# Optimization experiments

Measured on AMD Instinct MI355X. Metric: run time of the kernel, lower is better.

## Reference

```python
import jax, jax.numpy as jnp
import numpy as np

K = 20
EPS = 1e-5
NEG_SLOPE = 0.2


def knn(x, k):
    # x: [B, C, N] -> idx [B, N, k] of nearest neighbors (negative sq-dist topk)
    inner = -2.0 * jnp.einsum('bcn,bcm->bnm', x, x)
    xx = jnp.sum(x * x, axis=1)  # [B, N]
    d = -xx[:, :, None] - inner - xx[:, None, :]
    return jax.lax.top_k(d, k)[1]


def get_graph_feature(x, k):
    # x: [B, C, N] -> [B, 2C, N, k]
    idx = knn(x, k)
    xt = jnp.transpose(x, (0, 2, 1))            # [B, N, C]
    feat = jax.vmap(lambda a, i: a[i])(xt, idx)  # [B, N, k, C]
    center = xt[:, :, None, :]
    out = jnp.concatenate([feat - center, jnp.broadcast_to(center, feat.shape)], axis=-1)
    return jnp.transpose(out, (0, 3, 1, 2))


def conv_bn_lrelu(x, w, g, b):
    # 1x1 conv + BatchNorm2d (batch stats, training mode) + LeakyReLU(0.2)
    y = jnp.einsum('oc,bcnk->bonk', w, x)
    mu = jnp.mean(y, axis=(0, 2, 3), keepdims=True)
    var = jnp.mean((y - mu) ** 2, axis=(0, 2, 3), keepdims=True)
    y = (y - mu) * jax.lax.rsqrt(var + EPS)
    y = y * g[None, :, None, None] + b[None, :, None, None]
    return jnp.where(y >= 0, y, NEG_SLOPE * y)


def lrelu(y):
    return jnp.where(y >= 0, y, NEG_SLOPE * y)


def setup_inputs() -> dict:
    key = jax.random.key(0)
    ks = jax.random.split(key, 24)
    B, N = 8, 4096
    d = {}
    d['x'] = jax.random.normal(ks[0], (B, 3, N), dtype=jnp.float32)
    def wconv(k_, o, c):
        return jax.random.normal(k_, (o, c), dtype=jnp.float32) * (1.0 / np.sqrt(c))
    d['w1'] = wconv(ks[1], 32, 6)
    d['g1'] = 1.0 + 0.1 * jax.random.normal(ks[2], (32,), dtype=jnp.float32)
    d['b1'] = 0.1 * jax.random.normal(ks[3], (32,), dtype=jnp.float32)
    d['w2'] = wconv(ks[4], 64, 70)
    d['g2'] = 1.0 + 0.1 * jax.random.normal(ks[5], (64,), dtype=jnp.float32)
    d['b2'] = 0.1 * jax.random.normal(ks[6], (64,), dtype=jnp.float32)
    d['wd1'] = wconv(ks[7], 64, 64)
    d['gd1'] = 1.0 + 0.1 * jax.random.normal(ks[8], (64,), dtype=jnp.float32)
    d['bd1'] = 0.1 * jax.random.normal(ks[9], (64,), dtype=jnp.float32)
    d['wd2'] = wconv(ks[10], 64, 128)
    d['gd2'] = 1.0 + 0.1 * jax.random.normal(ks[11], (64,), dtype=jnp.float32)
    d['bd2'] = 0.1 * jax.random.normal(ks[12], (64,), dtype=jnp.float32)
    d['W2d'] = jax.random.normal(ks[13], (128, 128), dtype=jnp.float32) * (1.0 / np.sqrt(128))
    d['b2d'] = 0.1 * jax.random.normal(ks[14], (128,), dtype=jnp.float32)
    d['W3d'] = jax.random.normal(ks[15], (64, 128), dtype=jnp.float32) * (1.0 / np.sqrt(128))
    d['b3d'] = 0.1 * jax.random.normal(ks[16], (64,), dtype=jnp.float32)
    d['W4d'] = jax.random.normal(ks[17], (11, 64), dtype=jnp.float32) * (1.0 / np.sqrt(64))
    d['b4d'] = 0.1 * jax.random.normal(ks[18], (11,), dtype=jnp.float32)
    return d


def reference(x, w1, g1, b1, w2, g2, b2, wd1, gd1, bd1, wd2, gd2, bd2,
              W2d, b2d, W3d, b3d, W4d, b4d):
    x1_gf = get_graph_feature(x, K)                    # [B, 6, N, k]
    x1_max = jnp.max(conv_bn_lrelu(x1_gf, w1, g1, b1), axis=-1)  # [B, 32, N]
    x2_gf = jnp.concatenate([x1_gf, get_graph_feature(x1_max, K)], axis=1)  # [B, 70, N, k]
    x2_max = jnp.max(conv_bn_lrelu(x2_gf, w2, g2, b2), axis=-1)  # [B, 64, N]
    xd1 = jnp.max(conv_bn_lrelu(get_graph_feature(x1_max, K), wd1, gd1, bd1), axis=-1)  # [B, 64, N]
    xd2 = jnp.max(conv_bn_lrelu(get_graph_feature(x2_max, K), wd2, gd2, bd2), axis=-1)  # [B, 64, N]
    h = jnp.concatenate([xd1, xd2], axis=1)            # [B, 128, N]
    h = h.reshape(1, -1, 128)                          # faithful row-major view
    h = jnp.mean(h, axis=1)                            # [1, 128]
    h = lrelu(h @ W2d.T + b2d)
    h = lrelu(h @ W3d.T + b3d)
    return lrelu(h @ W4d.T + b4d)                      # [1, 11]
```

## Files before the change

### kernel.cpp

```cpp
#include <hip/hip_runtime.h>

#define BB 8
#define NN 4096
#define KK 20
constexpr float EPSV = 1e-5f;
constexpr float SLOPE = 0.2f;

typedef __bf16 bfrag __attribute__((ext_vector_type(8)));
typedef float floatx4 __attribute__((ext_vector_type(4)));
typedef unsigned short us4 __attribute__((ext_vector_type(4)));

__device__ __forceinline__ float lrelu(float v) { return v >= 0.f ? v : SLOPE * v; }

__device__ __forceinline__ unsigned short bf16rn(float f) {
    unsigned int u = __float_as_uint(f);
    return (unsigned short)((u + 0x7FFFu + ((u >> 16) & 1u)) >> 16);
}
__device__ __forceinline__ float bf16up(unsigned short h) {
    return __uint_as_float(((unsigned int)h) << 16);
}

__global__ void zero_kernel(float* p, int n) {
    int i = blockIdx.x * 256 + threadIdx.x;
    if (i < n) p[i] = 0.f;
}

template<int C>
__global__ void halfnorm_kernel(const float* __restrict__ src, float* __restrict__ hng) {
    int n = blockIdx.x * 256 + threadIdx.x;
    int b = blockIdx.y;
    float s = 0.f;
    #pragma unroll
    for (int c = 0; c < C; c++) { float v = src[(b * C + c) * NN + n]; s += v * v; }
    hng[b * NN + n] = 0.5f * s;
}

template<int C>
__global__ __launch_bounds__(256) void knn_kernel(const float* __restrict__ src,
                                                  const float* __restrict__ hng,
                                                  int* __restrict__ idx) {
    constexpr int SK = (C == 3) ? 40 : (2 * C + 8);
    __shared__ unsigned short qpack[64 * SK];
    __shared__ unsigned short cpack[64 * SK];
    __shared__ float hn[64];
    __shared__ float pv[64 * 65];
    __shared__ unsigned short pidx[64 * 66];
    __shared__ float tau[64];
    __shared__ int   cnt[64];

    const int b = blockIdx.y;
    const int q0 = blockIdx.x * 64;
    const int tid = threadIdx.x;
    const int lane = tid & 63;
    const int wv = tid >> 6;
    const int wr = (wv >> 1) * 32;
    const int wc = (wv & 1) * 32;
    const int fl = lane & 15;
    const int fq = lane >> 4;

    if (C == 3) {
        for (int i = tid; i < 64 * 20; i += 256) {
            int r = i / 20, k = 12 + i % 20;
            qpack[r * SK + k] = 0; cpack[r * SK + k] = 0;
        }
        if (tid < 64) {
            int q = tid;
            #pragma unroll
            for (int c = 0; c < 3; c++) {
                float v = src[(b * 3 + c) * NN + q0 + q];
                unsigned short h = bf16rn(v);
                unsigned short l = bf16rn(v - bf16up(h));
                qpack[q * SK + c] = h;  qpack[q * SK + 3 + c] = l;
                qpack[q * SK + 6 + c] = h;  qpack[q * SK + 9 + c] = l;
            }
        }
    } else {
        for (int t = 0; t < C / 16; t++) {
            int i = t * 256 + tid;
            int c4 = (i >> 6) * 4, m = i & 63;
            us4 hv, lv;
            #pragma unroll
            for (int j = 0; j < 4; j++) {
                float v = src[(b * C + c4 + j) * NN + q0 + m];
                unsigned short h = bf16rn(v);
                hv[j] = h;
                lv[j] = bf16rn(v - bf16up(h));
            }
            *(us4*)(&qpack[m * SK + c4]) = hv;
            *(us4*)(&qpack[m * SK + C + c4]) = lv;
        }
    }
    if (tid < 64) { tau[tid] = -3.4e38f; cnt[tid] = 0; }

    float tv[20]; int ti[20];
    #pragma unroll
    for (int k = 0; k < 20; k++) { tv[k] = -3.4e38f; ti[k] = 0; }
    __syncthreads();

    for (int ch = 0; ch < 64; ch++) {
        const int m0 = ch * 64;
        if (C == 3) {
            if (tid < 64) {
                int m = tid;
                #pragma unroll
                for (int c = 0; c < 3; c++) {
                    float v = src[(b * 3 + c) * NN + m0 + m];
                    unsigned short h = bf16rn(v);
                    unsigned short l = bf16rn(v - bf16up(h));
                    cpack[m * SK + c] = h;  cpack[m * SK + 3 + c] = l;
                    cpack[m * SK + 6 + c] = l;  cpack[m * SK + 9 + c] = h;
                }
            }
        } else {
            for (int t = 0; t < C / 16; t++) {
                int i = t * 256 + tid;
                int c4 = (i >> 6) * 4, m = i & 63;
                us4 hv, lv;
                #pragma unroll
                for (int j = 0; j < 4; j++) {
                    float v = src[(b * C + c4 + j) * NN + m0 + m];
                    unsigned short h = bf16rn(v);
                    hv[j] = h;
                    lv[j] = bf16rn(v - bf16up(h));
                }
                *(us4*)(&cpack[m * SK + c4]) = hv;
                *(us4*)(&cpack[m * SK + C + c4]) = lv;
            }
        }
        if (tid < 16) *(float4*)(hn + tid * 4) = *(const float4*)(hng + b * NN + m0 + tid * 4);
        __syncthreads();

        floatx4 acc[2][2];
        #pragma unroll
        for (int r2 = 0; r2 < 2; r2++)
            #pragma unroll
            for (int c2 = 0; c2 < 2; c2++)
                acc[r2][c2] = (floatx4)(0.f);

        if (C == 3) {
            #pragma unroll
            for (int r2 = 0; r2 < 2; r2++) {
                bfrag a = *(const bfrag*)(&qpack[(wr + r2 * 16 + fl) * SK + fq * 8]);
                #pragma unroll
                for (int c2 = 0; c2 < 2; c2++) {
                    bfrag bm = *(const bfrag*)(&cpack[(wc + c2 * 16 + fl) * SK + fq * 8]);
                    acc[r2][c2] = __builtin_amdgcn_mfma_f32_16x16x32_bf16(a, bm, acc[r2][c2], 0, 0, 0);
                }
            }
        } else {
            #pragma unroll
            for (int kk = 0; kk < C / 32; kk++) {
                const int kb = kk * 32 + fq * 8;
                bfrag ah[2], al[2], bh[2], bl[2];
                #pragma unroll
                for (int r2 = 0; r2 < 2; r2++) {
                    ah[r2] = *(const bfrag*)(&qpack[(wr + r2 * 16 + fl) * SK + kb]);
                    al[r2] = *(const bfrag*)(&qpack[(wr + r2 * 16 + fl) * SK + C + kb]);
                }
                #pragma unroll
                for (int c2 = 0; c2 < 2; c2++) {
                    bh[c2] = *(const bfrag*)(&cpack[(wc + c2 * 16 + fl) * SK + kb]);
                    bl[c2] = *(const bfrag*)(&cpack[(wc + c2 * 16 + fl) * SK + C + kb]);
                }
                #pragma unroll
                for (int r2 = 0; r2 < 2; r2++)
                    #pragma unroll
                    for (int c2 = 0; c2 < 2; c2++) {
                        acc[r2][c2] = __builtin_amdgcn_mfma_f32_16x16x32_bf16(ah[r2], bh[c2], acc[r2][c2], 0, 0, 0);
                        acc[r2][c2] = __builtin_amdgcn_mfma_f32_16x16x32_bf16(ah[r2], bl[c2], acc[r2][c2], 0, 0, 0);
                        acc[r2][c2] = __builtin_amdgcn_mfma_f32_16x16x32_bf16(al[r2], bh[c2], acc[r2][c2], 0, 0, 0);
                        acc[r2][c2] = __builtin_amdgcn_mfma_f32_16x16x32_bf16(al[r2], bl[c2], acc[r2][c2], 0, 0, 0);
                    }
            }
        }

        float hnv[2];
        #pragma unroll
        for (int c2 = 0; c2 < 2; c2++) hnv[c2] = hn[wc + c2 * 16 + fl];
        #pragma unroll
        for (int r2 = 0; r2 < 2; r2++) {
            float4 t4 = *(const float4*)(&tau[wr + r2 * 16 + fq * 4]);
            float ta[4] = {t4.x, t4.y, t4.z, t4.w};
            #pragma unroll
            for (int c2 = 0; c2 < 2; c2++) {
                #pragma unroll
                for (int reg = 0; reg < 4; reg++) {
                    float s = acc[r2][c2][reg] - hnv[c2];
                    if (s > ta[reg]) {
                        int q = wr + r2 * 16 + fq * 4 + reg;
                        int p = atomicAdd(&cnt[q], 1);
                        pv[q * 65 + p] = s;
                        pidx[q * 66 + p] = (unsigned short)(m0 + wc + c2 * 16 + fl);
                    }
                }
            }
        }
        __syncthreads();

        if (tid < 64) {
            int n = cnt[tid];
            for (int t = 0; t < n; t++) {
                float v = pv[tid * 65 + t];
                if (v > tv[0]) {
                    tv[0] = v; ti[0] = (int)pidx[tid * 66 + t];
                    #pragma unroll
                    for (int j = 0; j < 19; j++) {
                        if (tv[j] > tv[j + 1]) {
                            float a = tv[j]; tv[j] = tv[j + 1]; tv[j + 1] = a;
                            int bi = ti[j]; ti[j] = ti[j + 1]; ti[j + 1] = bi;
                        }
                    }
                }
            }
            cnt[tid] = 0;
            tau[tid] = tv[0];
        }
        __syncthreads();
    }

    if (tid < 64) {
        #pragma unroll
        for (int k = 0; k < 20; k++)
            idx[(b * NN + q0 + tid) * KK + k] = ti[k];
    }
}

template<int COUT>
__global__ void precompute_kernel(const float* __restrict__ src, int C,
                                  const float* __restrict__ w, int CIN, int wd_off, int wc_off,
                                  float* __restrict__ G, float* __restrict__ H,
                                  int initG, int initH) {
    constexpr int MY = 256 / COUT;
    extern __shared__ float lds[];
    float* wd = lds;
    float* wc = lds + C * COUT;
    const int b = blockIdx.y;
    const int tid = threadIdx.y * COUT + threadIdx.x;
    for (int i = tid; i < C * COUT; i += 256) {
        int c = i / COUT, o = i % COUT;
        float a  = w[o * CIN + wd_off + c];
        float cc = w[o * CIN + wc_off + c];
        wd[i] = a;
        wc[i] = cc - a;
    }
    __syncthreads();
    const int o = threadIdx.x;
    for (int it = 0; it < COUT / 4; it++) {
        int m = blockIdx.x * 64 + it * MY + threadIdx.y;
        float g = 0.f, h = 0.f;
        for (int c = 0; c < C; c++) {
            float s = src[(b * C + c) * NN + m];
            g += wd[c * COUT + o] * s;
            h += wc[c * COUT + o] * s;
        }
        int gi = (b * NN + m) * COUT + o;
        if (initG) G[gi] = g; else G[gi] += g;
        if (initH) H[gi] = h; else H[gi] += h;
    }
}

template<int COUT, int GROUPS>
__global__ void conv_stats_kernel(const float* __restrict__ G1, const int* __restrict__ idx1,
                                  const float* __restrict__ G2, const int* __restrict__ idx2,
                                  const float* __restrict__ H, float* __restrict__ stats,
                                  float* __restrict__ MaxY, float* __restrict__ MinY) {
    constexpr int NY = 256 / COUT;
    const int b = blockIdx.y;
    const int o = threadIdx.x;
    const int n = blockIdx.x * NY + threadIdx.y;
    const int base = b * NN + n;
    const float h = H[base * COUT + o];
    float s1 = 0.f, s2 = 0.f;
    float gx = -3.4e38f, gn = 3.4e38f;
    #pragma unroll
    for (int k = 0; k < KK; k++) {
        int i1 = idx1[base * KK + k];
        float g = G1[(b * NN + i1) * COUT + o];
        if (GROUPS == 2) {
            int i2 = idx2[base * KK + k];
            g += G2[(b * NN + i2) * COUT + o];
        }
        float y = g + h;
        s1 += y;
        s2 += y * y;
        gx = fmaxf(gx, g);
        gn = fminf(gn, g);
    }
    MaxY[base * COUT + o] = gx + h;
    MinY[base * COUT + o] = gn + h;

    __shared__ float ls[2 * COUT];
    if (threadIdx.y == 0) { ls[o] = 0.f; ls[COUT + o] = 0.f; }
    __syncthreads();
    atomicAdd(&ls[o], s1);
    atomicAdd(&ls[COUT + o], s2);
    __syncthreads();
    if (threadIdx.y == 0) {
        atomicAdd(&stats[o], ls[o]);
        atomicAdd(&stats[64 + o], ls[COUT + o]);
    }
}

__global__ void finalize_kernel(const float* __restrict__ g, const float* __restrict__ bb,
                                float* __restrict__ stats, int cout, float invP) {
    int o = threadIdx.x;
    if (o >= cout) return;
    float mu  = stats[o] * invP;
    float var = stats[64 + o] * invP - mu * mu;
    float sc  = g[o] * rsqrtf(var + EPSV);
    stats[128 + o] = sc;
    stats[192 + o] = bb[o] - mu * sc;
}

__global__ void apply_kernel(const float* __restrict__ MaxY, const float* __restrict__ MinY,
                             const float* __restrict__ stats, float* __restrict__ out, int cout) {
    int e = blockIdx.x * 256 + threadIdx.x;
    int total = BB * cout * NN;
    if (e >= total) return;
    int n = e & (NN - 1);
    int o = (e >> 12) % cout;
    int b = e / (NN * cout);
    float sc = stats[128 + o], sh = stats[192 + o];
    int si = (b * NN + n) * cout + o;
    float v = (sc >= 0.f) ? MaxY[si] : MinY[si];
    out[e] = lrelu(sc * v + sh);
}

__global__ void mean_kernel(const float* __restrict__ xd1, const float* __restrict__ xd2,
                            float* __restrict__ hsum) {
    __shared__ float bins[128];
    const int tid = threadIdx.x;
    if (tid < 128) bins[tid] = 0.f;
    __syncthreads();
    const int half = BB * 64 * NN;
    const int stride = gridDim.x * 256;
    for (int e = blockIdx.x * 256 + tid; e < half; e += stride)
        atomicAdd(&bins[e & 127], xd1[e]);
    for (int e = blockIdx.x * 256 + tid; e < half; e += stride)
        atomicAdd(&bins[e & 127], xd2[e]);
    __syncthreads();
    if (tid < 128) atomicAdd(&hsum[tid], bins[tid]);
}

__global__ void head_kernel(const float* __restrict__ hsum,
                            const float* __restrict__ W2d, const float* __restrict__ b2d,
                            const float* __restrict__ W3d, const float* __restrict__ b3d,
                            const float* __restrict__ W4d, const float* __restrict__ b4d,
                            float* __restrict__ out) {
    __shared__ float h[128], t1[128], t2[64];
    const int t = threadIdx.x;
    h[t] = hsum[t] * (1.f / 32768.f);
    __syncthreads();
    float a = b2d[t];
    for (int j = 0; j < 128; j++) a += W2d[t * 128 + j] * h[j];
    t1[t] = lrelu(a);
    __syncthreads();
    if (t < 64) {
        float a2 = b3d[t];
        for (int j = 0; j < 128; j++) a2 += W3d[t * 128 + j] * t1[j];
        t2[t] = lrelu(a2);
    }
    __syncthreads();
    if (t < 11) {
        float a3 = b4d[t];
        for (int j = 0; j < 64; j++) a3 += W4d[t * 64 + j] * t2[j];
        out[t] = lrelu(a3);
    }
}

extern "C" void kernel_launch(void* const* d_in, const int* in_sizes, int n_in,
                              void* d_out, int out_size, void* d_ws, size_t ws_size,
                              hipStream_t stream) {
    const float* x   = (const float*)d_in[0];
    const float* w1  = (const float*)d_in[1];
    const float* g1  = (const float*)d_in[2];
    const float* b1  = (const float*)d_in[3];
    const float* w2  = (const float*)d_in[4];
    const float* g2  = (const float*)d_in[5];
    const float* b2  = (const float*)d_in[6];
    const float* wd1 = (const float*)d_in[7];
    const float* gd1 = (const float*)d_in[8];
    const float* bd1 = (const float*)d_in[9];
    const float* wd2 = (const float*)d_in[10];
    const float* gd2 = (const float*)d_in[11];
    const float* bd2 = (const float*)d_in[12];
    const float* W2d = (const float*)d_in[13];
    const float* b2d = (const float*)d_in[14];
    const float* W3d = (const float*)d_in[15];
    const float* b3d = (const float*)d_in[16];
    const float* W4d = (const float*)d_in[17];
    const float* b4d = (const float*)d_in[18];
    float* out = (float*)d_out;

    char* ws = (char*)d_ws;
    size_t off = 0;
    auto alloc = [&](size_t bytes) { char* p = ws + off; off += (bytes + 255) & ~size_t(255); return p; };
    int*   idx1  = (int*)  alloc(BB * NN * KK * 4);
    int*   idx2  = (int*)  alloc(BB * NN * KK * 4);
    int*   idx3  = (int*)  alloc(BB * NN * KK * 4);
    float* x1m   = (float*)alloc(BB * 32 * NN * 4);
    float* x2m   = (float*)alloc(BB * 64 * NN * 4);
    float* xd1   = (float*)alloc(BB * 64 * NN * 4);
    float* xd2   = (float*)alloc(BB * 64 * NN * 4);
    float* G1    = (float*)alloc((size_t)BB * NN * 64 * 4);
    float* G2    = (float*)alloc((size_t)BB * NN * 64 * 4);
    float* H     = (float*)alloc((size_t)BB * NN * 64 * 4);
    float* MaxY  = (float*)alloc((size_t)BB * NN * 64 * 4);
    float* MinY  = (float*)alloc((size_t)BB * NN * 64 * 4);
    float* stats = (float*)alloc(256 * 4);
    float* hsum  = (float*)alloc(128 * 4);
    float* hng   = (float*)alloc(BB * NN * 4);

    const float invP = 1.f / (float)(BB * NN * KK);
    const dim3 knn_grid(NN / 64, BB);
    const dim3 hn_grid(NN / 256, BB);

    zero_kernel<<<1, 256, 0, stream>>>(hsum, 128);

    halfnorm_kernel<3><<<hn_grid, 256, 0, stream>>>(x, hng);
    knn_kernel<3><<<knn_grid, 256, 0, stream>>>(x, hng, idx1);

    zero_kernel<<<1, 256, 0, stream>>>(stats, 128);
    precompute_kernel<32><<<dim3(NN / 64, BB), dim3(32, 8), 2 * 3 * 32 * 4, stream>>>(
        x, 3, w1, 6, 0, 3, G1, H, 1, 1);
    conv_stats_kernel<32, 1><<<dim3(NN / 8, BB), dim3(32, 8), 0, stream>>>(
        G1, idx1, nullptr, nullptr, H, stats, MaxY, MinY);
    finalize_kernel<<<1, 64, 0, stream>>>(g1, b1, stats, 32, invP);
    apply_kernel<<<(BB * 32 * NN + 255) / 256, 256, 0, stream>>>(MaxY, MinY, stats, x1m, 32);

    halfnorm_kernel<32><<<hn_grid, 256, 0, stream>>>(x1m, hng);
    knn_kernel<32><<<knn_grid, 256, 0, stream>>>(x1m, hng, idx2);

    zero_kernel<<<1, 256, 0, stream>>>(stats, 128);
    precompute_kernel<64><<<dim3(NN / 64, BB), dim3(64, 4), 2 * 3 * 64 * 4, stream>>>(
        x, 3, w2, 70, 0, 3, G1, H, 1, 1);
    precompute_kernel<64><<<dim3(NN / 64, BB), dim3(64, 4), 2 * 32 * 64 * 4, stream>>>(
        x1m, 32, w2, 70, 6, 38, G2, H, 1, 0);
    conv_stats_kernel<64, 2><<<dim3(NN / 4, BB), dim3(64, 4), 0, stream>>>(
        G1, idx1, G2, idx2, H, stats, MaxY, MinY);
    finalize_kernel<<<1, 64, 0, stream>>>(g2, b2, stats, 64, invP);
    apply_kernel<<<(BB * 64 * NN + 255) / 256, 256, 0, stream>>>(MaxY, MinY, stats, x2m, 64);

    zero_kernel<<<1, 256, 0, stream>>>(stats, 128);
    precompute_kernel<64><<<dim3(NN / 64, BB), dim3(64, 4), 2 * 32 * 64 * 4, stream>>>(
        x1m, 32, wd1, 64, 0, 32, G1, H, 1, 1);
    conv_stats_kernel<64, 1><<<dim3(NN / 4, BB), dim3(64, 4), 0, stream>>>(
        G1, idx2, nullptr, nullptr, H, stats, MaxY, MinY);
    finalize_kernel<<<1, 64, 0, stream>>>(gd1, bd1, stats, 64, invP);
    apply_kernel<<<(BB * 64 * NN + 255) / 256, 256, 0, stream>>>(MaxY, MinY, stats, xd1, 64);

    halfnorm_kernel<64><<<hn_grid, 256, 0, stream>>>(x2m, hng);
    knn_kernel<64><<<knn_grid, 256, 0, stream>>>(x2m, hng, idx3);

    zero_kernel<<<1, 256, 0, stream>>>(stats, 128);
    precompute_kernel<64><<<dim3(NN / 64, BB), dim3(64, 4), 2 * 64 * 64 * 4, stream>>>(
        x2m, 64, wd2, 128, 0, 64, G1, H, 1, 1);
    conv_stats_kernel<64, 1><<<dim3(NN / 4, BB), dim3(64, 4), 0, stream>>>(
        G1, idx3, nullptr, nullptr, H, stats, MaxY, MinY);
    finalize_kernel<<<1, 64, 0, stream>>>(gd2, bd2, stats, 64, invP);
    apply_kernel<<<(BB * 64 * NN + 255) / 256, 256, 0, stream>>>(MaxY, MinY, stats, xd2, 64);

    mean_kernel<<<1024, 256, 0, stream>>>(xd1, xd2, hsum);
    head_kernel<<<1, 128, 0, stream>>>(hsum, W2d, b2d, W3d, b3d, W4d, b4d, out);
}
```

Baseline: 1.758 ms.

## Split KNN top-k insertion across four threads per query and prefetch chunks

After: 1.745 ms. Within noise of the previous version (-0.7%).

```diff
diff --git a/kernel.cpp b/kernel.cpp
--- a/kernel.cpp
+++ b/kernel.cpp
@@ -40,12 +40,13 @@
                                                   const float* __restrict__ hng,
                                                   int* __restrict__ idx) {
     constexpr int SK = (C == 3) ? 40 : (2 * C + 8);
+    constexpr int PFN = (C == 3) ? 3 : (C / 4);
     __shared__ unsigned short qpack[64 * SK];
     __shared__ unsigned short cpack[64 * SK];
     __shared__ float hn[64];
     __shared__ float pv[64 * 65];
     __shared__ unsigned short pidx[64 * 66];
-    __shared__ float tau[64];
+    __shared__ float tau[256];
     __shared__ int   cnt[64];
 
     const int b = blockIdx.y;
@@ -57,6 +58,11 @@
     const int wc = (wv & 1) * 32;
     const int fl = lane & 15;
     const int fq = lane >> 4;
+    const int dq = tid & 63;
+    const int ds = tid >> 6;
+
+    float pf[PFN];
+    float4 hnp;
 
     if (C == 3) {
         for (int i = tid; i < 64 * 20; i += 256) {
@@ -90,12 +96,28 @@
             *(us4*)(&qpack[m * SK + C + c4]) = lv;
         }
     }
-    if (tid < 64) { tau[tid] = -3.4e38f; cnt[tid] = 0; }
+    tau[tid] = -3.4e38f;
 
     float tv[20]; int ti[20];
     #pragma unroll
     for (int k = 0; k < 20; k++) { tv[k] = -3.4e38f; ti[k] = 0; }
-    __syncthreads();
+
+    if (C == 3) {
+        if (tid < 64) {
+            #pragma unroll
+            for (int c = 0; c < 3; c++) pf[c] = src[(b * 3 + c) * NN + tid];
+        }
+    } else {
+        #pragma unroll
+        for (int t = 0; t < C / 16; t++) {
+            int i = t * 256 + tid;
+            int c4 = (i >> 6) * 4, m = i & 63;
+            #pragma unroll
+            for (int j = 0; j < 4; j++)
+                pf[t * 4 + j] = src[(b * C + c4 + j) * NN + m];
+        }
+    }
+    if (tid < 16) hnp = *(const float4*)(hng + b * NN + tid * 4);
 
     for (int ch = 0; ch < 64; ch++) {
         const int m0 = ch * 64;
@@ -104,7 +126,7 @@
                 int m = tid;
                 #pragma unroll
                 for (int c = 0; c < 3; c++) {
-                    float v = src[(b * 3 + c) * NN + m0 + m];
+                    float v = pf[c];
                     unsigned short h = bf16rn(v);
                     unsigned short l = bf16rn(v - bf16up(h));
                     cpack[m * SK + c] = h;  cpack[m * SK + 3 + c] = l;
@@ -112,13 +134,14 @@
                 }
             }
         } else {
+            #pragma unroll
             for (int t = 0; t < C / 16; t++) {
                 int i = t * 256 + tid;
                 int c4 = (i >> 6) * 4, m = i & 63;
                 us4 hv, lv;
                 #pragma unroll
                 for (int j = 0; j < 4; j++) {
-                    float v = src[(b * C + c4 + j) * NN + m0 + m];
+                    float v = pf[t * 4 + j];
                     unsigned short h = bf16rn(v);
                     hv[j] = h;
                     lv[j] = bf16rn(v - bf16up(h));
@@ -127,7 +150,28 @@
                 *(us4*)(&cpack[m * SK + C + c4]) = lv;
             }
         }
-        if (tid < 16) *(float4*)(hn + tid * 4) = *(const float4*)(hng + b * NN + m0 + tid * 4);
+        if (tid < 16) *(float4*)(hn + tid * 4) = hnp;
+        if (tid < 64) cnt[tid] = 0;
+
+        if (ch + 1 < 64) {
+            const int m1 = m0 + 64;
+            if (C == 3) {
+                if (tid < 64) {
+                    #pragma unroll
+                    for (int c = 0; c < 3; c++) pf[c] = src[(b * 3 + c) * NN + m1 + tid];
+                }
+            } else {
+                #pragma unroll
+                for (int t = 0; t < C / 16; t++) {
+                    int i = t * 256 + tid;
+                    int c4 = (i >> 6) * 4, m = i & 63;
+                    #pragma unroll
+                    for (int j = 0; j < 4; j++)
+                        pf[t * 4 + j] = src[(b * C + c4 + j) * NN + m1 + m];
+                }
+            }
+            if (tid < 16) hnp = *(const float4*)(hng + b * NN + m1 + tid * 4);
+        }
         __syncthreads();
 
         floatx4 acc[2][2];
@@ -179,15 +223,22 @@
         for (int c2 = 0; c2 < 2; c2++) hnv[c2] = hn[wc + c2 * 16 + fl];
         #pragma unroll
         for (int r2 = 0; r2 < 2; r2++) {
-            float4 t4 = *(const float4*)(&tau[wr + r2 * 16 + fq * 4]);
-            float ta[4] = {t4.x, t4.y, t4.z, t4.w};
+            const int qq = wr + r2 * 16 + fq * 4;
+            float4 t0 = *(const float4*)(&tau[qq]);
+            float4 t1 = *(const float4*)(&tau[64 + qq]);
+            float4 t2 = *(const float4*)(&tau[128 + qq]);
+            float4 t3 = *(const float4*)(&tau[192 + qq]);
+            float ta[4] = { fmaxf(fmaxf(t0.x, t1.x), fmaxf(t2.x, t3.x)),
+                            fmaxf(fmaxf(t0.y, t1.y), fmaxf(t2.y, t3.y)),
+                            fmaxf(fmaxf(t0.z, t1.z), fmaxf(t2.z, t3.z)),
+                            fmaxf(fmaxf(t0.w, t1.w), fmaxf(t2.w, t3.w)) };
             #pragma unroll
             for (int c2 = 0; c2 < 2; c2++) {
                 #pragma unroll
                 for (int reg = 0; reg < 4; reg++) {
                     float s = acc[r2][c2][reg] - hnv[c2];
                     if (s > ta[reg]) {
-                        int q = wr + r2 * 16 + fq * 4 + reg;
+                        int q = qq + reg;
                         int p = atomicAdd(&cnt[q], 1);
                         pv[q * 65 + p] = s;
                         pidx[q * 66 + p] = (unsigned short)(m0 + wc + c2 * 16 + fl);
@@ -197,12 +248,12 @@
         }
         __syncthreads();
 
-        if (tid < 64) {
-            int n = cnt[tid];
-            for (int t = 0; t < n; t++) {
-                float v = pv[tid * 65 + t];
+        {
+            int n = cnt[dq];
+            for (int t = ds; t < n; t += 4) {
+                float v = pv[dq * 65 + t];
                 if (v > tv[0]) {
-                    tv[0] = v; ti[0] = (int)pidx[tid * 66 + t];
+                    tv[0] = v; ti[0] = (int)pidx[dq * 66 + t];
                     #pragma unroll
                     for (int j = 0; j < 19; j++) {
                         if (tv[j] > tv[j + 1]) {
@@ -212,13 +263,33 @@
                     }
                 }
             }
-            cnt[tid] = 0;
             tau[tid] = tv[0];
         }
         __syncthreads();
     }
 
+    if (ds > 0) {
+        #pragma unroll
+        for (int k = 0; k < 20; k++) {
+            pv[dq * 65 + (ds - 1) * 20 + k] = tv[k];
+            pidx[dq * 66 + (ds - 1) * 20 + k] = (unsigned short)ti[k];
+        }
+    }
+    __syncthreads();
     if (tid < 64) {
+        for (int t = 0; t < 60; t++) {
+            float v = pv[tid * 65 + t];
+            if (v > tv[0]) {
+                tv[0] = v; ti[0] = (int)pidx[tid * 66 + t];
+                #pragma unroll
+                for (int j = 0; j < 19; j++) {
+                    if (tv[j] > tv[j + 1]) {
+                        float a = tv[j]; tv[j] = tv[j + 1]; tv[j + 1] = a;
+                        int bi = ti[j]; ti[j] = ti[j + 1]; ti[j + 1] = bi;
+                    }
+                }
+            }
+        }
         #pragma unroll
         for (int k = 0; k < 20; k++)
             idx[(b * NN + q0 + tid) * KK + k] = ti[k];
```

## Prepack bf16 split operands, prefetch candidate tiles, and parallelize kNN top-k selection

Applied to the files above, without the earlier changes.

Result: slower. 2.665 ms (+51.6%).

```diff
diff --git a/kernel.cpp b/kernel.cpp
--- a/kernel.cpp
+++ b/kernel.cpp
@@ -9,6 +9,7 @@
 typedef __bf16 bfrag __attribute__((ext_vector_type(8)));
 typedef float floatx4 __attribute__((ext_vector_type(4)));
 typedef unsigned short us4 __attribute__((ext_vector_type(4)));
+typedef unsigned short us8 __attribute__((ext_vector_type(8)));
 
 __device__ __forceinline__ float lrelu(float v) { return v >= 0.f ? v : SLOPE * v; }
 
@@ -36,17 +37,44 @@
 }
 
 template<int C>
+__global__ void pack_kernel(const float* __restrict__ src, unsigned short* __restrict__ pk) {
+    constexpr int SK = 2 * C + 8;
+    const int b = blockIdx.y;
+    const int m0 = blockIdx.x * 64;
+    const int tid = threadIdx.x;
+    for (int i = tid; i < 64 * (C / 4); i += 256) {
+        int m = i & 63;
+        int c4 = (i >> 6) * 4;
+        us4 hv, lv;
+        #pragma unroll
+        for (int j = 0; j < 4; j++) {
+            float v = src[(b * C + c4 + j) * NN + m0 + m];
+            unsigned short h = bf16rn(v);
+            hv[j] = h;
+            lv[j] = bf16rn(v - bf16up(h));
+        }
+        *(us4*)(&pk[(size_t)(b * NN + m0 + m) * SK + c4]) = hv;
+        *(us4*)(&pk[(size_t)(b * NN + m0 + m) * SK + C + c4]) = lv;
+    }
+    for (int i = tid; i < 64 * 2; i += 256) {
+        int m = i >> 1, p = (i & 1) * 4;
+        *(us4*)(&pk[(size_t)(b * NN + m0 + m) * SK + 2 * C + p]) = (us4)(0);
+    }
+}
+
+template<int C>
 __global__ __launch_bounds__(256) void knn_kernel(const float* __restrict__ src,
+                                                  const unsigned short* __restrict__ pk,
                                                   const float* __restrict__ hng,
                                                   int* __restrict__ idx) {
     constexpr int SK = (C == 3) ? 40 : (2 * C + 8);
-    __shared__ unsigned short qpack[64 * SK];
-    __shared__ unsigned short cpack[64 * SK];
+    constexpr int UNITS = 8 * SK;
+    constexpr int PF = (C == 3) ? 1 : ((UNITS + 255) / 256);
+    __shared__ __attribute__((aligned(16))) unsigned short qpack[64 * SK];
+    __shared__ __attribute__((aligned(16))) unsigned short cpack[64 * SK];
+    __shared__ __attribute__((aligned(16))) float sv[64 * 68];
     __shared__ float hn[64];
-    __shared__ float pv[64 * 65];
-    __shared__ unsigned short pidx[64 * 66];
-    __shared__ float tau[64];
-    __shared__ int   cnt[64];
+    __shared__ unsigned short midx3[(C == 3) ? 64 * 60 : 1];
 
     const int b = blockIdx.y;
     const int q0 = blockIdx.x * 64;
@@ -57,6 +85,16 @@
     const int wc = (wv & 1) * 32;
     const int fl = lane & 15;
     const int fq = lane >> 4;
+    const int dq = tid & 63;
+    const int ds = tid >> 6;
+
+    float tv[20]; int ti[20];
+    #pragma unroll
+    for (int k = 0; k < 20; k++) { tv[k] = -3.4e38f; ti[k] = 0; }
+
+    us8 pf[PF];
+    float pf3[3];
+    float hnf = 0.f;
 
     if (C == 3) {
         for (int i = tid; i < 64 * 20; i += 256) {
@@ -64,72 +102,47 @@
             qpack[r * SK + k] = 0; cpack[r * SK + k] = 0;
         }
         if (tid < 64) {
-            int q = tid;
             #pragma unroll
             for (int c = 0; c < 3; c++) {
-                float v = src[(b * 3 + c) * NN + q0 + q];
+                float v = src[(b * 3 + c) * NN + q0 + tid];
                 unsigned short h = bf16rn(v);
                 unsigned short l = bf16rn(v - bf16up(h));
-                qpack[q * SK + c] = h;  qpack[q * SK + 3 + c] = l;
-                qpack[q * SK + 6 + c] = h;  qpack[q * SK + 9 + c] = l;
-            }
+                qpack[tid * SK + c] = h;  qpack[tid * SK + 3 + c] = l;
+                qpack[tid * SK + 6 + c] = h;  qpack[tid * SK + 9 + c] = l;
+                float v2 = src[(b * 3 + c) * NN + tid];
+                unsigned short h2 = bf16rn(v2);
+                unsigned short l2 = bf16rn(v2 - bf16up(h2));
+                cpack[tid * SK + c] = h2;  cpack[tid * SK + 3 + c] = l2;
+                cpack[tid * SK + 6 + c] = l2;  cpack[tid * SK + 9 + c] = h2;
+            }
+            #pragma unroll
+            for (int c = 0; c < 3; c++) pf3[c] = src[(b * 3 + c) * NN + 64 + tid];
         }
     } else {
-        for (int t = 0; t < C / 16; t++) {
-            int i = t * 256 + tid;
-            int c4 = (i >> 6) * 4, m = i & 63;
-            us4 hv, lv;
-            #pragma unroll
-            for (int j = 0; j < 4; j++) {
-                float v = src[(b * C + c4 + j) * NN + q0 + m];
-                unsigned short h = bf16rn(v);
-                hv[j] = h;
-                lv[j] = bf16rn(v - bf16up(h));
-            }
-            *(us4*)(&qpack[m * SK + c4]) = hv;
-            *(us4*)(&qpack[m * SK + C + c4]) = lv;
-        }
-    }
-    if (tid < 64) { tau[tid] = -3.4e38f; cnt[tid] = 0; }
-
-    float tv[20]; int ti[20];
-    #pragma unroll
-    for (int k = 0; k < 20; k++) { tv[k] = -3.4e38f; ti[k] = 0; }
+        const unsigned short* pkq = pk + (size_t)(b * NN + q0) * SK;
+        const unsigned short* pk0 = pk + (size_t)(b * NN) * SK;
+        #pragma unroll
+        for (int r = 0; r < PF; r++) {
+            int i = r * 256 + tid;
+            if (i < UNITS) {
+                *(us8*)(qpack + i * 8) = *(const us8*)(pkq + i * 8);
+                *(us8*)(cpack + i * 8) = *(const us8*)(pk0 + i * 8);
+            }
+        }
+        const unsigned short* pk1 = pk + (size_t)(b * NN + 64) * SK;
+        #pragma unroll
+        for (int r = 0; r < PF; r++) {
+            int i = r * 256 + tid;
+            if (i < UNITS) pf[r] = *(const us8*)(pk1 + i * 8);
+        }
+    }
+    if (tid < 64) {
+        hn[tid] = hng[b * NN + tid];
+        hnf = hng[b * NN + 64 + tid];
+    }
     __syncthreads();
 
     for (int ch = 0; ch < 64; ch++) {
-        const int m0 = ch * 64;
-        if (C == 3) {
-            if (tid < 64) {
-                int m = tid;
-                #pragma unroll
-                for (int c = 0; c < 3; c++) {
-                    float v = src[(b * 3 + c) * NN + m0 + m];
-                    unsigned short h = bf16rn(v);
-                    unsigned short l = bf16rn(v - bf16up(h));
-                    cpack[m * SK + c] = h;  cpack[m * SK + 3 + c] = l;
-                    cpack[m * SK + 6 + c] = l;  cpack[m * SK + 9 + c] = h;
-                }
-            }
-        } else {
-            for (int t = 0; t < C / 16; t++) {
-                int i = t * 256 + tid;
-                int c4 = (i >> 6) * 4, m = i & 63;
-                us4 hv, lv;
-                #pragma unroll
-                for (int j = 0; j < 4; j++) {
-                    float v = src[(b * C + c4 + j) * NN + m0 + m];
-                    unsigned short h = bf16rn(v);
-                    hv[j] = h;
-                    lv[j] = bf16rn(v - bf16up(h));
-                }
-                *(us4*)(&cpack[m * SK + c4]) = hv;
-                *(us4*)(&cpack[m * SK + C + c4]) = lv;
-            }
-        }
-        if (tid < 16) *(float4*)(hn + tid * 4) = *(const float4*)(hng + b * NN + m0 + tid * 4);
-        __syncthreads();
-
         floatx4 acc[2][2];
         #pragma unroll
         for (int r2 = 0; r2 < 2; r2++)
@@ -174,35 +187,68 @@
             }
         }
 
-        float hnv[2];
-        #pragma unroll
-        for (int c2 = 0; c2 < 2; c2++) hnv[c2] = hn[wc + c2 * 16 + fl];
         #pragma unroll
         for (int r2 = 0; r2 < 2; r2++) {
-            float4 t4 = *(const float4*)(&tau[wr + r2 * 16 + fq * 4]);
-            float ta[4] = {t4.x, t4.y, t4.z, t4.w};
+            const int qb = wr + r2 * 16 + fq * 4;
             #pragma unroll
             for (int c2 = 0; c2 < 2; c2++) {
-                #pragma unroll
-                for (int reg = 0; reg < 4; reg++) {
-                    float s = acc[r2][c2][reg] - hnv[c2];
-                    if (s > ta[reg]) {
-                        int q = wr + r2 * 16 + fq * 4 + reg;
-                        int p = atomicAdd(&cnt[q], 1);
-                        pv[q * 65 + p] = s;
-                        pidx[q * 66 + p] = (unsigned short)(m0 + wc + c2 * 16 + fl);
+                const int m = wc + c2 * 16 + fl;
+                const float h = hn[m];
+                float4 s;
+                s.x = acc[r2][c2][0] - h;
+                s.y = acc[r2][c2][1] - h;
+                s.z = acc[r2][c2][2] - h;
+                s.w = acc[r2][c2][3] - h;
+                *(float4*)(&sv[m * 68 + qb]) = s;
+            }
+        }
+        __syncthreads();
+
+        if (ch + 1 < 64) {
+            if (C == 3) {
+                if (tid < 64) {
+                    #pragma unroll
+                    for (int c = 0; c < 3; c++) {
+                        float v = pf3[c];
+                        unsigned short h = bf16rn(v);
+                        unsigned short l = bf16rn(v - bf16up(h));
+                        cpack[tid * SK + c] = h;  cpack[tid * SK + 3 + c] = l;
+                        cpack[tid * SK + 6 + c] = l;  cpack[tid * SK + 9 + c] = h;
                     }
                 }
-            }
-        }
-        __syncthreads();
-
-        if (tid < 64) {
-            int n = cnt[tid];
-            for (int t = 0; t < n; t++) {
-                float v = pv[tid * 65 + t];
+            } else {
+                #pragma unroll
+                for (int r = 0; r < PF; r++) {
+                    int i = r * 256 + tid;
+                    if (i < UNITS) *(us8*)(cpack + i * 8) = pf[r];
+                }
+            }
+            if (tid < 64) hn[tid] = hnf;
+        }
+        if (ch + 2 < 64) {
+            const int m2 = (ch + 2) * 64;
+            if (C == 3) {
+                if (tid < 64) {
+                    #pragma unroll
+                    for (int c = 0; c < 3; c++) pf3[c] = src[(b * 3 + c) * NN + m2 + tid];
+                }
+            } else {
+                const unsigned short* pkn = pk + (size_t)(b * NN + m2) * SK;
+                #pragma unroll
+                for (int r = 0; r < PF; r++) {
+                    int i = r * 256 + tid;
+                    if (i < UNITS) pf[r] = *(const us8*)(pkn + i * 8);
+                }
+            }
+            if (tid < 64) hnf = hng[b * NN + m2 + tid];
+        }
+        {
+            const int mbase = ch * 64;
+            for (int r = 0; r < 16; r++) {
+                const int t = ds + r * 4;
+                float v = sv[t * 68 + dq];
                 if (v > tv[0]) {
-                    tv[0] = v; ti[0] = (int)pidx[tid * 66 + t];
+                    tv[0] = v; ti[0] = mbase + t;
                     #pragma unroll
                     for (int j = 0; j < 19; j++) {
                         if (tv[j] > tv[j + 1]) {
@@ -212,16 +258,36 @@
                     }
                 }
             }
-            cnt[tid] = 0;
-            tau[tid] = tv[0];
         }
         __syncthreads();
     }
 
+    unsigned short* midx = (C == 3) ? midx3 : (unsigned short*)qpack;
+    if (ds > 0) {
+        #pragma unroll
+        for (int k = 0; k < 20; k++) {
+            sv[((ds - 1) * 20 + k) * 68 + dq] = tv[k];
+            midx[dq * 60 + (ds - 1) * 20 + k] = (unsigned short)ti[k];
+        }
+    }
+    __syncthreads();
     if (tid < 64) {
+        for (int t = 0; t < 60; t++) {
+            float v = sv[t * 68 + dq];
+            if (v > tv[0]) {
+                tv[0] = v; ti[0] = (int)midx[dq * 60 + t];
+                #pragma unroll
+                for (int j = 0; j < 19; j++) {
+                    if (tv[j] > tv[j + 1]) {
+                        float a = tv[j]; tv[j] = tv[j + 1]; tv[j + 1] = a;
+                        int bi = ti[j]; ti[j] = ti[j + 1]; ti[j + 1] = bi;
+                    }
+                }
+            }
+        }
         #pragma unroll
         for (int k = 0; k < 20; k++)
-            idx[(b * NN + q0 + tid) * KK + k] = ti[k];
+            idx[(b * NN + q0 + dq) * KK + k] = ti[k];
     }
 }
 
@@ -411,6 +477,8 @@
     float* hsum  = (float*)alloc(128 * 4);
     float* hng   = (float*)alloc(BB * NN * 4);
 
+    unsigned short* pkbuf = (unsigned short*)MaxY;
+
     const float invP = 1.f / (float)(BB * NN * KK);
     const dim3 knn_grid(NN / 64, BB);
     const dim3 hn_grid(NN / 256, BB);
@@ -418,7 +486,7 @@
     zero_kernel<<<1, 256, 0, stream>>>(hsum, 128);
 
     halfnorm_kernel<3><<<hn_grid, 256, 0, stream>>>(x, hng);
-    knn_kernel<3><<<knn_grid, 256, 0, stream>>>(x, hng, idx1);
+    knn_kernel<3><<<knn_grid, 256, 0, stream>>>(x, nullptr, hng, idx1);
 
     zero_kernel<<<1, 256, 0, stream>>>(stats, 128);
     precompute_kernel<32><<<dim3(NN / 64, BB), dim3(32, 8), 2 * 3 * 32 * 4, stream>>>(
@@ -428,8 +496,9 @@
     finalize_kernel<<<1, 64, 0, stream>>>(g1, b1, stats, 32, invP);
     apply_kernel<<<(BB * 32 * NN + 255) / 256, 256, 0, stream>>>(MaxY, MinY, stats, x1m, 32);
 
+    pack_kernel<32><<<dim3(NN / 64, BB), 256, 0, stream>>>(x1m, pkbuf);
     halfnorm_kernel<32><<<hn_grid, 256, 0, stream>>>(x1m, hng);
-    knn_kernel<32><<<knn_grid, 256, 0, stream>>>(x1m, hng, idx2);
+    knn_kernel<32><<<knn_grid, 256, 0, stream>>>(x1m, pkbuf, hng, idx2);
 
     zero_kernel<<<1, 256, 0, stream>>>(stats, 128);
     precompute_kernel<64><<<dim3(NN / 64, BB), dim3(64, 4), 2 * 3 * 64 * 4, stream>>>(
@@ -449,8 +518,9 @@
     finalize_kernel<<<1, 64, 0, stream>>>(gd1, bd1, stats, 64, invP);
     apply_kernel<<<(BB * 64 * NN + 255) / 256, 256, 0, stream>>>(MaxY, MinY, stats, xd1, 64);
 
+    pack_kernel<64><<<dim3(NN / 64, BB), 256, 0, stream>>>(x2m, pkbuf);
     halfnorm_kernel<64><<<hn_grid, 256, 0, stream>>>(x2m, hng);
-    knn_kernel<64><<<knn_grid, 256, 0, stream>>>(x2m, hng, idx3);
+    knn_kernel<64><<<knn_grid, 256, 0, stream>>>(x2m, pkbuf, hng, idx3);
 
     zero_kernel<<<1, 256, 0, stream>>>(stats, 128);
     precompute_kernel<64><<<dim3(NN / 64, BB), dim3(64, 4), 2 * 64 * 64 * 4, stream>>>(
```

## Prepack bf16 hi/lo features globally and software-pipeline candidate tiles in kNN

Applied to the files above, without the earlier changes.

After: 2.110 ms. +20.1%, slower.

```diff
diff --git a/kernel.cpp b/kernel.cpp
--- a/kernel.cpp
+++ b/kernel.cpp
@@ -9,6 +9,7 @@
 typedef __bf16 bfrag __attribute__((ext_vector_type(8)));
 typedef float floatx4 __attribute__((ext_vector_type(4)));
 typedef unsigned short us4 __attribute__((ext_vector_type(4)));
+typedef unsigned short us8 __attribute__((ext_vector_type(8)));
 
 __device__ __forceinline__ float lrelu(float v) { return v >= 0.f ? v : SLOPE * v; }
 
@@ -36,192 +37,242 @@
 }
 
 template<int C>
+__global__ void pack_kernel(const float* __restrict__ src, unsigned short* __restrict__ pk) {
+    constexpr int SK = 2 * C + 8;
+    const int b = blockIdx.y;
+    const int m0 = blockIdx.x * 64;
+    const int tid = threadIdx.x;
+    for (int i = tid; i < 64 * (C / 4); i += 256) {
+        int m = i & 63;
+        int c4 = (i >> 6) * 4;
+        us4 hv, lv;
+        #pragma unroll
+        for (int j = 0; j < 4; j++) {
+            float v = src[(b * C + c4 + j) * NN + m0 + m];
+            unsigned short h = bf16rn(v);
+            hv[j] = h;
+            lv[j] = bf16rn(v - bf16up(h));
+        }
+        *(us4*)(&pk[(size_t)(b * NN + m0 + m) * SK + c4]) = hv;
+        *(us4*)(&pk[(size_t)(b * NN + m0 + m) * SK + C + c4]) = lv;
+    }
+    for (int i = tid; i < 64 * 2; i += 256) {
+        int m = i >> 1, p = (i & 1) * 4;
+        *(us4*)(&pk[(size_t)(b * NN + m0 + m) * SK + 2 * C + p]) = (us4)(0);
+    }
+}
+
+__global__ void pack3_kernel(const float* __restrict__ src, unsigned short* __restrict__ pk) {
+    const int b = blockIdx.y;
+    const int m = blockIdx.x * 256 + threadIdx.x;
+    us8 w0, w1;
+    #pragma unroll
+    for (int j = 0; j < 8; j++) { w0[j] = 0; w1[j] = 0; }
+    unsigned short row[12];
+    #pragma unroll
+    for (int c = 0; c < 3; c++) {
+        float v = src[(b * 3 + c) * NN + m];
+        unsigned short h = bf16rn(v);
+        unsigned short l = bf16rn(v - bf16up(h));
+        row[c] = h; row[3 + c] = l; row[6 + c] = l; row[9 + c] = h;
+    }
+    #pragma unroll
+    for (int j = 0; j < 8; j++) w0[j] = row[j];
+    #pragma unroll
+    for (int j = 0; j < 4; j++) w1[j] = row[8 + j];
+    unsigned short* dst = pk + (size_t)(b * NN + m) * 40;
+    us8 z;
+    #pragma unroll
+    for (int j = 0; j < 8; j++) z[j] = 0;
+    *(us8*)(dst) = w0;
+    *(us8*)(dst + 8) = w1;
+    *(us8*)(dst + 16) = z;
+    *(us8*)(dst + 24) = z;
+    *(us8*)(dst + 32) = z;
+}
+
+template<int C>
 __global__ __launch_bounds__(256) void knn_kernel(const float* __restrict__ src,
+                                                  const unsigned short* __restrict__ pk,
                                                   const float* __restrict__ hng,
                                                   int* __restrict__ idx) {
     constexpr int SK = (C == 3) ? 40 : (2 * C + 8);
-    __shared__ unsigned short qpack[64 * SK];
-    __shared__ unsigned short cpack[64 * SK];
+    constexpr int UNITS = 8 * SK;
+    constexpr int PFC = (UNITS + 191) / 192;
+    constexpr int KKN = (C == 3) ? 1 : (C / 32);
+    __shared__ __attribute__((aligned(16))) unsigned short cpack[64 * SK];
+    __shared__ float pv[32 * 65];
+    __shared__ unsigned short pidx[32 * 66];
     __shared__ float hn[64];
-    __shared__ float pv[64 * 65];
-    __shared__ unsigned short pidx[64 * 66];
-    __shared__ float tau[64];
-    __shared__ int   cnt[64];
+    __shared__ float tau[32];
+    __shared__ int cnt[32];
+    __shared__ unsigned short qls[(C == 3) ? 32 * 40 : 2];
 
     const int b = blockIdx.y;
-    const int q0 = blockIdx.x * 64;
+    const int q0 = blockIdx.x * 32;
     const int tid = threadIdx.x;
     const int lane = tid & 63;
     const int wv = tid >> 6;
-    const int wr = (wv >> 1) * 32;
+    const int wr = (wv >> 1) * 16;
     const int wc = (wv & 1) * 32;
     const int fl = lane & 15;
     const int fq = lane >> 4;
-
+    const int ci = tid - 64;
+
+    float tv[20]; int ti[20];
+    #pragma unroll
+    for (int k = 0; k < 20; k++) { tv[k] = -3.4e38f; ti[k] = 0; }
+
+    bfrag qah[KKN], qal[KKN];
     if (C == 3) {
-        for (int i = tid; i < 64 * 20; i += 256) {
+        for (int i = tid; i < 32 * 20; i += 256) {
             int r = i / 20, k = 12 + i % 20;
-            qpack[r * SK + k] = 0; cpack[r * SK + k] = 0;
-        }
-        if (tid < 64) {
-            int q = tid;
+            qls[r * 40 + k] = 0;
+        }
+        if (tid < 32) {
             #pragma unroll
             for (int c = 0; c < 3; c++) {
-                float v = src[(b * 3 + c) * NN + q0 + q];
+                float v = src[(b * 3 + c) * NN + q0 + tid];
                 unsigned short h = bf16rn(v);
                 unsigned short l = bf16rn(v - bf16up(h));
-                qpack[q * SK + c] = h;  qpack[q * SK + 3 + c] = l;
-                qpack[q * SK + 6 + c] = h;  qpack[q * SK + 9 + c] = l;
+                qls[tid * 40 + c] = h;  qls[tid * 40 + 3 + c] = l;
+                qls[tid * 40 + 6 + c] = h;  qls[tid * 40 + 9 + c] = l;
             }
         }
     } else {
-        for (int t = 0; t < C / 16; t++) {
-            int i = t * 256 + tid;
-            int c4 = (i >> 6) * 4, m = i & 63;
-            us4 hv, lv;
-            #pragma unroll
-            for (int j = 0; j < 4; j++) {
-                float v = src[(b * C + c4 + j) * NN + q0 + m];
-                unsigned short h = bf16rn(v);
-                hv[j] = h;
-                lv[j] = bf16rn(v - bf16up(h));
-            }
-            *(us4*)(&qpack[m * SK + c4]) = hv;
-            *(us4*)(&qpack[m * SK + C + c4]) = lv;
-        }
-    }
-    if (tid < 64) { tau[tid] = -3.4e38f; cnt[tid] = 0; }
-
-    float tv[20]; int ti[20];
-    #pragma unroll
-    for (int k = 0; k < 20; k++) { tv[k] = -3.4e38f; ti[k] = 0; }
-    __syncthreads();
+        const unsigned short* qr = pk + (size_t)(b * NN + q0 + wr + fl) * SK + fq * 8;
+        #pragma unroll
+        for (int kk = 0; kk < KKN; kk++) {
+            qah[kk] = *(const bfrag*)(qr + kk * 32);
+            qal[kk] = *(const bfrag*)(qr + C + kk * 32);
+        }
+    }
+
+    {
+        const unsigned short* p0 = pk + (size_t)(b * NN) * SK;
+        for (int i = tid; i < UNITS; i += 256)
+            *(us8*)(cpack + i * 8) = *(const us8*)(p0 + i * 8);
+    }
+    us8 pf[PFC];
+    if (wv > 0) {
+        const unsigned short* p1 = pk + (size_t)(b * NN + 64) * SK;
+        #pragma unroll
+        for (int r = 0; r < PFC; r++) {
+            int u = r * 192 + ci;
+            if (u < UNITS) pf[r] = *(const us8*)(p1 + u * 8);
+        }
+    }
+    float hnf = 0.f;
+    if (wv == 0) {
+        hn[lane] = hng[b * NN + lane];
+        hnf = hng[b * NN + 64 + lane];
+        if (lane < 32) { tau[lane] = -3.4e38f; cnt[lane] = 0; }
+    }
+    __syncthreads();
+
+    bfrag qa3;
+    if (C == 3) qa3 = *(const bfrag*)(&qls[(wr + fl) * 40 + fq * 8]);
 
     for (int ch = 0; ch < 64; ch++) {
-        const int m0 = ch * 64;
-        if (C == 3) {
-            if (tid < 64) {
-                int m = tid;
-                #pragma unroll
-                for (int c = 0; c < 3; c++) {
-                    float v = src[(b * 3 + c) * NN + m0 + m];
-                    unsigned short h = bf16rn(v);
-                    unsigned short l = bf16rn(v - bf16up(h));
-                    cpack[m * SK + c] = h;  cpack[m * SK + 3 + c] = l;
-                    cpack[m * SK + 6 + c] = l;  cpack[m * SK + 9 + c] = h;
-                }
-            }
-        } else {
-            for (int t = 0; t < C / 16; t++) {
-                int i = t * 256 + tid;
-                int c4 = (i >> 6) * 4, m = i & 63;
-                us4 hv, lv;
-                #pragma unroll
-                for (int j = 0; j < 4; j++) {
-                    float v = src[(b * C + c4 + j) * NN + m0 + m];
-                    unsigned short h = bf16rn(v);
-                    hv[j] = h;
-                    lv[j] = bf16rn(v - bf16up(h));
-                }
-                *(us4*)(&cpack[m * SK + c4]) = hv;
-                *(us4*)(&cpack[m * SK + C + c4]) = lv;
-            }
-        }
-        if (tid < 16) *(float4*)(hn + tid * 4) = *(const float4*)(hng + b * NN + m0 + tid * 4);
-        __syncthreads();
-
-        floatx4 acc[2][2];
-        #pragma unroll
-        for (int r2 = 0; r2 < 2; r2++)
-            #pragma unroll
-            for (int c2 = 0; c2 < 2; c2++)
-                acc[r2][c2] = (floatx4)(0.f);
+        floatx4 acc[2];
+        acc[0] = (floatx4)(0.f);
+        acc[1] = (floatx4)(0.f);
 
         if (C == 3) {
             #pragma unroll
-            for (int r2 = 0; r2 < 2; r2++) {
-                bfrag a = *(const bfrag*)(&qpack[(wr + r2 * 16 + fl) * SK + fq * 8]);
-                #pragma unroll
-                for (int c2 = 0; c2 < 2; c2++) {
-                    bfrag bm = *(const bfrag*)(&cpack[(wc + c2 * 16 + fl) * SK + fq * 8]);
-                    acc[r2][c2] = __builtin_amdgcn_mfma_f32_16x16x32_bf16(a, bm, acc[r2][c2], 0, 0, 0);
-                }
+            for (int c2 = 0; c2 < 2; c2++) {
+                bfrag bm = *(const bfrag*)(&cpack[(wc + c2 * 16 + fl) * SK + fq * 8]);
+                acc[c2] = __builtin_amdgcn_mfma_f32_16x16x32_bf16(qa3, bm, acc[c2], 0, 0, 0);
             }
         } else {
             #pragma unroll
-            for (int kk = 0; kk < C / 32; kk++) {
+            for (int kk = 0; kk < KKN; kk++) {
                 const int kb = kk * 32 + fq * 8;
-                bfrag ah[2], al[2], bh[2], bl[2];
-                #pragma unroll
-                for (int r2 = 0; r2 < 2; r2++) {
-                    ah[r2] = *(const bfrag*)(&qpack[(wr + r2 * 16 + fl) * SK + kb]);
-                    al[r2] = *(const bfrag*)(&qpack[(wr + r2 * 16 + fl) * SK + C + kb]);
-                }
+                bfrag bh[2], bl[2];
                 #pragma unroll
                 for (int c2 = 0; c2 < 2; c2++) {
                     bh[c2] = *(const bfrag*)(&cpack[(wc + c2 * 16 + fl) * SK + kb]);
                     bl[c2] = *(const bfrag*)(&cpack[(wc + c2 * 16 + fl) * SK + C + kb]);
                 }
                 #pragma unroll
-                for (int r2 = 0; r2 < 2; r2++)
-                    #pragma unroll
-                    for (int c2 = 0; c2 < 2; c2++) {
-                        acc[r2][c2] = __builtin_amdgcn_mfma_f32_16x16x32_bf16(ah[r2], bh[c2], acc[r2][c2], 0, 0, 0);
-                        acc[r2][c2] = __builtin_amdgcn_mfma_f32_16x16x32_bf16(ah[r2], bl[c2], acc[r2][c2], 0, 0, 0);
-                        acc[r2][c2] = __builtin_amdgcn_mfma_f32_16x16x32_bf16(al[r2], bh[c2], acc[r2][c2], 0, 0, 0);
-                        acc[r2][c2] = __builtin_amdgcn_mfma_f32_16x16x32_bf16(al[r2], bl[c2], acc[r2][c2], 0, 0, 0);
-                    }
-            }
-        }
-
-        float hnv[2];
-        #pragma unroll
-        for (int c2 = 0; c2 < 2; c2++) hnv[c2] = hn[wc + c2 * 16 + fl];
-        #pragma unroll
-        for (int r2 = 0; r2 < 2; r2++) {
-            float4 t4 = *(const float4*)(&tau[wr + r2 * 16 + fq * 4]);
-            float ta[4] = {t4.x, t4.y, t4.z, t4.w};
+                for (int c2 = 0; c2 < 2; c2++) {
+                    acc[c2] = __builtin_amdgcn_mfma_f32_16x16x32_bf16(qah[kk], bh[c2], acc[c2], 0, 0, 0);
+                    acc[c2] = __builtin_amdgcn_mfma_f32_16x16x32_bf16(qah[kk], bl[c2], acc[c2], 0, 0, 0);
+                    acc[c2] = __builtin_amdgcn_mfma_f32_16x16x32_bf16(qal[kk], bh[c2], acc[c2], 0, 0, 0);
+                    acc[c2] = __builtin_amdgcn_mfma_f32_16x16x32_bf16(qal[kk], bl[c2], acc[c2], 0, 0, 0);
+                }
+            }
+        }
+
+        {
+            const int m0 = ch * 64;
+            const float hnv0 = hn[wc + fl];
+            const float hnv1 = hn[wc + 16 + fl];
+            float4 t4 = *(const float4*)(&tau[wr + fq * 4]);
+            float ta[4] = { t4.x, t4.y, t4.z, t4.w };
             #pragma unroll
             for (int c2 = 0; c2 < 2; c2++) {
+                const float hv = c2 ? hnv1 : hnv0;
+                const int mm = m0 + wc + c2 * 16 + fl;
                 #pragma unroll
                 for (int reg = 0; reg < 4; reg++) {
-                    float s = acc[r2][c2][reg] - hnv[c2];
+                    float s = acc[c2][reg] - hv;
                     if (s > ta[reg]) {
-                        int q = wr + r2 * 16 + fq * 4 + reg;
+                        int q = wr + fq * 4 + reg;
                         int p = atomicAdd(&cnt[q], 1);
                         pv[q * 65 + p] = s;
-                        pidx[q * 66 + p] = (unsigned short)(m0 + wc + c2 * 16 + fl);
+                        pidx[q * 66 + p] = (unsigned short)mm;
                     }
                 }
             }
         }
         __syncthreads();
 
-        if (tid < 64) {
-            int n = cnt[tid];
-            for (int t = 0; t < n; t++) {
-                float v = pv[tid * 65 + t];
-                if (v > tv[0]) {
-                    tv[0] = v; ti[0] = (int)pidx[tid * 66 + t];
-                    #pragma unroll
-                    for (int j = 0; j < 19; j++) {
-                        if (tv[j] > tv[j + 1]) {
-                            float a = tv[j]; tv[j] = tv[j + 1]; tv[j + 1] = a;
-                            int bi = ti[j]; ti[j] = ti[j + 1]; ti[j + 1] = bi;
+        if (wv == 0) {
+            if (ch + 1 < 64) hn[lane] = hnf;
+            if (ch + 2 < 64) hnf = hng[b * NN + (ch + 2) * 64 + lane];
+            if (lane < 32) {
+                int n = cnt[lane];
+                for (int t = 0; t < n; t++) {
+                    float v = pv[lane * 65 + t];
+                    if (v > tv[0]) {
+                        tv[0] = v; ti[0] = (int)pidx[lane * 66 + t];
+                        #pragma unroll
+                        for (int j = 0; j < 19; j++) {
+                            if (tv[j] > tv[j + 1]) {
+                                float a = tv[j]; tv[j] = tv[j + 1]; tv[j + 1] = a;
+                                int bi = ti[j]; ti[j] = ti[j + 1]; ti[j + 1] = bi;
+                            }
                         }
                     }
                 }
-            }
-            cnt[tid] = 0;
-            tau[tid] = tv[0];
+                cnt[lane] = 0;
+                tau[lane] = tv[0];
+            }
+        } else {
+            if (ch + 1 < 64) {
+                #pragma unroll
+                for (int r = 0; r < PFC; r++) {
+                    int u = r * 192 + ci;
+                    if (u < UNITS) *(us8*)(cpack + u * 8) = pf[r];
+                }
+            }
+            if (ch + 2 < 64) {
+                const unsigned short* pn = pk + (size_t)(b * NN + (ch + 2) * 64) * SK;
+                #pragma unroll
+                for (int r = 0; r < PFC; r++) {
+                    int u = r * 192 + ci;
+                    if (u < UNITS) pf[r] = *(const us8*)(pn + u * 8);
+                }
+            }
         }
         __syncthreads();
     }
 
-    if (tid < 64) {
+    if (wv == 0 && lane < 32) {
         #pragma unroll
         for (int k = 0; k < 20; k++)
-            idx[(b * NN + q0 + tid) * KK + k] = ti[k];
+            idx[(b * NN + q0 + lane) * KK + k] = ti[k];
     }
 }
 
@@ -411,14 +462,17 @@
     float* hsum  = (float*)alloc(128 * 4);
     float* hng   = (float*)alloc(BB * NN * 4);
 
+    unsigned short* pkbuf = (unsigned short*)MaxY;
+
     const float invP = 1.f / (float)(BB * NN * KK);
-    const dim3 knn_grid(NN / 64, BB);
+    const dim3 knn_grid(NN / 32, BB);
     const dim3 hn_grid(NN / 256, BB);
 
     zero_kernel<<<1, 256, 0, stream>>>(hsum, 128);
 
+    pack3_kernel<<<dim3(NN / 256, BB), 256, 0, stream>>>(x, pkbuf);
     halfnorm_kernel<3><<<hn_grid, 256, 0, stream>>>(x, hng);
-    knn_kernel<3><<<knn_grid, 256, 0, stream>>>(x, hng, idx1);
+    knn_kernel<3><<<knn_grid, 256, 0, stream>>>(x, pkbuf, hng, idx1);
 
     zero_kernel<<<1, 256, 0, stream>>>(stats, 128);
     precompute_kernel<32><<<dim3(NN / 64, BB), dim3(32, 8), 2 * 3 * 32 * 4, stream>>>(
@@ -428,8 +482,9 @@
     finalize_kernel<<<1, 64, 0, stream>>>(g1, b1, stats, 32, invP);
     apply_kernel<<<(BB * 32 * NN + 255) / 256, 256, 0, stream>>>(MaxY, MinY, stats, x1m, 32);
 
+    pack_kernel<32><<<dim3(NN / 64, BB), 256, 0, stream>>>(x1m, pkbuf);
     halfnorm_kernel<32><<<hn_grid, 256, 0, stream>>>(x1m, hng);
-    knn_kernel<32><<<knn_grid, 256, 0, stream>>>(x1m, hng, idx2);
+    knn_kernel<32><<<knn_grid, 256, 0, stream>>>(x1m, pkbuf, hng, idx2);
 
     zero_kernel<<<1, 256, 0, stream>>>(stats, 128);
     precompute_kernel<64><<<dim3(NN / 64, BB), dim3(64, 4), 2 * 3 * 64 * 4, stream>>>(
@@ -449,8 +504,9 @@
     finalize_kernel<<<1, 64, 0, stream>>>(gd1, bd1, stats, 64, invP);
     apply_kernel<<<(BB * 64 * NN + 255) / 256, 256, 0, stream>>>(MaxY, MinY, stats, xd1, 64);
 
+    pack_kernel<64><<<dim3(NN / 64, BB), 256, 0, stream>>>(x2m, pkbuf);
     halfnorm_kernel<64><<<hn_grid, 256, 0, stream>>>(x2m, hng);
-    knn_kernel<64><<<knn_grid, 256, 0, stream>>>(x2m, hng, idx3);
+    knn_kernel<64><<<knn_grid, 256, 0, stream>>>(x2m, pkbuf, hng, idx3);
 
     zero_kernel<<<1, 256, 0, stream>>>(stats, 128);
     precompute_kernel<64><<<dim3(NN / 64, BB), dim3(64, 4), 2 * 64 * 64 * 4, stream>>>(
```
